# Performance work log

Measured on AMD Instinct MI355X. Metric: run time of the kernel, lower is better.

The kernel has to match this reference:

```python
import jax, jax.numpy as jnp
import numpy as np


def setup_inputs() -> dict:
    key = jax.random.key(0)
    k1, k2 = jax.random.split(key)
    pred_pts = jax.random.normal(k1, (8, 3, 4096), dtype=jnp.float32)  # [B,3,N]
    gt_pts = jax.random.normal(k2, (8, 4096, 3), dtype=jnp.float32)    # [B,M,3]
    return {"pred_pts": pred_pts, "gt_pts": gt_pts}


def _chamfer(p, g):
    # p: [B,N,3], g: [B,M,3]
    # squared euclidean distance matrix via ||p||^2 + ||g||^2 - 2 p.g
    pn = jnp.sum(p * p, axis=-1)  # [B,N]
    gn = jnp.sum(g * g, axis=-1)  # [B,M]
    cross = jnp.einsum("bnd,bmd->bnm", p, g)  # [B,N,M]
    D = pn[:, :, None] + gn[:, None, :] - 2.0 * cross  # [B,N,M]
    dist1 = jnp.min(D, axis=2)  # [B,N] min over gt for each pred point
    dist2 = jnp.min(D, axis=1)  # [B,M] min over pred for each gt point
    return dist1, dist2


def reference(pred_pts, gt_pts):
    p = jnp.swapaxes(pred_pts, -2, -1).astype(jnp.float32)  # [B,N,3]
    g = gt_pts  # [B,M,3]
    dist1, dist2 = _chamfer(p, g)
    per_batch = jnp.mean(dist1, axis=1) + jnp.mean(dist2, axis=1)  # [B]
    loss = jnp.sum(per_batch) / gt_pts.shape[0]
    return loss
```

## Files before the change

### kernel.cpp

```cpp
#include <hip/hip_runtime.h>

typedef float f32x2 __attribute__((ext_vector_type(2)));

#define NPTS 4096
#define BATCH 8
#define BLK 256
#define P 8
#define NPAIR (P / 2)
#define CHUNK 256
#define NCHUNK (NPTS / CHUNK)
#define OWN_PER_BLK (BLK * P)
#define OWN_BLKS (NPTS / OWN_PER_BLK)
#define BLOCKS_PER_PASS (BATCH * OWN_BLKS * NCHUNK)
#define TOTAL_BLOCKS (2 * BLOCKS_PER_PASS)
#define HALF_OWN (BATCH * NPTS)
#define TOTAL_OWN (2 * HALF_OWN)
#define COMBINE_BLOCKS (TOTAL_OWN / BLK)

static __device__ __forceinline__ f32x2 splat2(float v) {
    f32x2 r; r.x = v; r.y = v; return r;
}

__global__ __launch_bounds__(BLK) void chamfer_partial_kernel(
    const float* __restrict__ pred,
    const float* __restrict__ gt,
    float* __restrict__ partial)
{
    __shared__ float4 s[CHUNK];

    const int bid  = blockIdx.x;
    const int pass = bid / BLOCKS_PER_PASS;
    int r = bid - pass * BLOCKS_PER_PASS;
    const int c = r % NCHUNK;
    r /= NCHUNK;
    const int b = r / OWN_BLKS;
    const int j = r - b * OWN_BLKS;
    const int t = threadIdx.x;

    const float* p = pred + (size_t)b * 3 * NPTS;
    const float* g = gt   + (size_t)b * NPTS * 3;
    const int cbase = c * CHUNK;

    {
        int i = t;
        if (pass == 0) {
            int gi = cbase + i;
            float gx = g[gi * 3 + 0], gy = g[gi * 3 + 1], gz = g[gi * 3 + 2];
            s[i] = make_float4(-2.f * gx, -2.f * gy, -2.f * gz,
                               fmaf(gx, gx, fmaf(gy, gy, gz * gz)));
        } else {
            int pi = cbase + i;
            float px = p[pi], py = p[NPTS + pi], pz = p[2 * NPTS + pi];
            s[i] = make_float4(-2.f * px, -2.f * py, -2.f * pz,
                               fmaf(px, px, fmaf(py, py, pz * pz)));
        }
    }

    f32x2 X[NPAIR], Y[NPAIR], Z[NPAIR], N2[NPAIR];
    #pragma unroll
    for (int k = 0; k < P; ++k) {
        int idx = j * OWN_PER_BLK + k * BLK + t;
        float x, y, z;
        if (pass == 0) {
            x = p[idx]; y = p[NPTS + idx]; z = p[2 * NPTS + idx];
        } else {
            x = g[idx * 3 + 0]; y = g[idx * 3 + 1]; z = g[idx * 3 + 2];
        }
        X[k >> 1][k & 1] = x;
        Y[k >> 1][k & 1] = y;
        Z[k >> 1][k & 1] = z;
        N2[k >> 1][k & 1] = fmaf(x, x, fmaf(y, y, z * z));
    }
    __syncthreads();

    f32x2 A[NPAIR], B[NPAIR];
    #pragma unroll
    for (int pk = 0; pk < NPAIR; ++pk) { A[pk] = splat2(3.4e38f); B[pk] = splat2(3.4e38f); }

    #pragma unroll 2
    for (int mm = 0; mm < CHUNK; mm += 2) {
        float4 q0 = s[mm + 0];
        float4 q1 = s[mm + 1];
        f32x2 q0x = splat2(q0.x), q0y = splat2(q0.y), q0z = splat2(q0.z), q0w = splat2(q0.w);
        f32x2 q1x = splat2(q1.x), q1y = splat2(q1.y), q1z = splat2(q1.z), q1w = splat2(q1.w);
        #pragma unroll
        for (int pk = 0; pk < NPAIR; ++pk) {
            f32x2 d0 = __builtin_elementwise_fma(X[pk], q0x,
                        __builtin_elementwise_fma(Y[pk], q0y,
                         __builtin_elementwise_fma(Z[pk], q0z, q0w)));
            A[pk] = __builtin_elementwise_min(A[pk], d0);
            f32x2 d1 = __builtin_elementwise_fma(X[pk], q1x,
                        __builtin_elementwise_fma(Y[pk], q1y,
                         __builtin_elementwise_fma(Z[pk], q1z, q1w)));
            B[pk] = __builtin_elementwise_min(B[pk], d1);
        }
    }

    #pragma unroll
    for (int pk = 0; pk < NPAIR; ++pk) {
        f32x2 mn = __builtin_elementwise_min(A[pk], B[pk]);
        #pragma unroll
        for (int h = 0; h < 2; ++h) {
            int k = 2 * pk + h;
            int idx = j * OWN_PER_BLK + k * BLK + t;
            int o = pass * HALF_OWN + b * NPTS + idx;
            partial[(size_t)c * TOTAL_OWN + o] = N2[pk][h] + mn[h];
        }
    }
}

__global__ __launch_bounds__(BLK) void chamfer_combine_kernel(
    const float* __restrict__ partial, float* __restrict__ bsum)
{
    __shared__ float red[BLK / 64];
    const int t = threadIdx.x;
    const int o = blockIdx.x * BLK + t;
    float v = 3.4e38f;
    #pragma unroll
    for (int c = 0; c < NCHUNK; ++c)
        v = fminf(v, partial[(size_t)c * TOTAL_OWN + o]);
    #pragma unroll
    for (int off = 32; off > 0; off >>= 1)
        v += __shfl_down(v, off, 64);
    if ((t & 63) == 0) red[t >> 6] = v;
    __syncthreads();
    if (t == 0) bsum[blockIdx.x] = red[0] + red[1] + red[2] + red[3];
}

__global__ __launch_bounds__(COMBINE_BLOCKS) void chamfer_final_kernel(
    const float* __restrict__ bsum, float* __restrict__ out)
{
    __shared__ float red[COMBINE_BLOCKS / 64];
    const int t = threadIdx.x;
    float v = bsum[t];
    #pragma unroll
    for (int off = 32; off > 0; off >>= 1)
        v += __shfl_down(v, off, 64);
    if ((t & 63) == 0) red[t >> 6] = v;
    __syncthreads();
    if (t == 0) {
        float s = 0.f;
        #pragma unroll
        for (int w = 0; w < COMBINE_BLOCKS / 64; ++w) s += red[w];
        out[0] = s * (1.0f / ((float)NPTS * (float)BATCH));
    }
}

extern "C" void kernel_launch(void* const* d_in, const int* in_sizes, int n_in,
                              void* d_out, int out_size, void* d_ws, size_t ws_size,
                              hipStream_t stream) {
    const float* pred = (const float*)d_in[0];
    const float* gt   = (const float*)d_in[1];
    float* out = (float*)d_out;

    float* partial = (float*)d_ws;
    float* bsum    = partial + (size_t)NCHUNK * TOTAL_OWN;

    chamfer_partial_kernel<<<TOTAL_BLOCKS, BLK, 0, stream>>>(pred, gt, partial);
    chamfer_combine_kernel<<<COMBINE_BLOCKS, BLK, 0, stream>>>(partial, bsum);
    chamfer_final_kernel<<<1, COMBINE_BLOCKS, 0, stream>>>(bsum, out);
}
```

Measured before the change: 33.42 us.

## Precompute pre-splatted point stream in global memory and drop LDS staging

```diff
diff --git a/kernel.cpp b/kernel.cpp
--- a/kernel.cpp
+++ b/kernel.cpp
@@ -6,7 +6,7 @@
 #define BATCH 8
 #define BLK 256
 #define P 8
-#define NPAIR (P / 2)
+#define NPAIR 4
 #define CHUNK 256
 #define NCHUNK (NPTS / CHUNK)
 #define OWN_PER_BLK (BLK * P)
@@ -16,18 +16,48 @@
 #define HALF_OWN (BATCH * NPTS)
 #define TOTAL_OWN (2 * HALF_OWN)
 #define COMBINE_BLOCKS (TOTAL_OWN / BLK)
+#define STREAM_PTS (BATCH * NPTS)
+#define STREAM_PAD 16
+
+struct Pt8 { f32x2 x, y, z, w; };
 
 static __device__ __forceinline__ f32x2 splat2(float v) {
     f32x2 r; r.x = v; r.y = v; return r;
 }
 
-__global__ __launch_bounds__(BLK) void chamfer_partial_kernel(
+__global__ __launch_bounds__(BLK) void chamfer_prep_kernel(
     const float* __restrict__ pred,
     const float* __restrict__ gt,
+    Pt8* __restrict__ sA, Pt8* __restrict__ sB)
+{
+    const int i = blockIdx.x * BLK + threadIdx.x;
+    const int b = i >> 12;
+    const int m = i & (NPTS - 1);
+
+    {
+        const float* gp = gt + ((size_t)b * NPTS + m) * 3;
+        float gx = gp[0], gy = gp[1], gz = gp[2];
+        Pt8 e;
+        e.x = splat2(-2.f * gx); e.y = splat2(-2.f * gy); e.z = splat2(-2.f * gz);
+        e.w = splat2(fmaf(gx, gx, fmaf(gy, gy, gz * gz)));
+        sA[i] = e;
+    }
+    {
+        const float* pp = pred + (size_t)b * 3 * NPTS;
+        float px = pp[m], py = pp[NPTS + m], pz = pp[2 * NPTS + m];
+        Pt8 e;
+        e.x = splat2(-2.f * px); e.y = splat2(-2.f * py); e.z = splat2(-2.f * pz);
+        e.w = splat2(fmaf(px, px, fmaf(py, py, pz * pz)));
+        sB[i] = e;
+    }
+}
+
+__global__ __launch_bounds__(BLK, 2) void chamfer_partial_kernel(
+    const float* __restrict__ pred,
+    const float* __restrict__ gt,
+    const Pt8* __restrict__ sA, const Pt8* __restrict__ sB,
     float* __restrict__ partial)
 {
-    __shared__ float4 s[CHUNK];
-
     const int bid  = blockIdx.x;
     const int pass = bid / BLOCKS_PER_PASS;
     int r = bid - pass * BLOCKS_PER_PASS;
@@ -39,22 +69,7 @@
 
     const float* p = pred + (size_t)b * 3 * NPTS;
     const float* g = gt   + (size_t)b * NPTS * 3;
-    const int cbase = c * CHUNK;
-
-    {
-        int i = t;
-        if (pass == 0) {
-            int gi = cbase + i;
-            float gx = g[gi * 3 + 0], gy = g[gi * 3 + 1], gz = g[gi * 3 + 2];
-            s[i] = make_float4(-2.f * gx, -2.f * gy, -2.f * gz,
-                               fmaf(gx, gx, fmaf(gy, gy, gz * gz)));
-        } else {
-            int pi = cbase + i;
-            float px = p[pi], py = p[NPTS + pi], pz = p[2 * NPTS + pi];
-            s[i] = make_float4(-2.f * px, -2.f * py, -2.f * pz,
-                               fmaf(px, px, fmaf(py, py, pz * pz)));
-        }
-    }
+    const Pt8* __restrict__ st = (pass == 0 ? sA : sB) + (size_t)b * NPTS + c * CHUNK;
 
     f32x2 X[NPAIR], Y[NPAIR], Z[NPAIR], N2[NPAIR];
     #pragma unroll
@@ -71,30 +86,32 @@
         Z[k >> 1][k & 1] = z;
         N2[k >> 1][k & 1] = fmaf(x, x, fmaf(y, y, z * z));
     }
-    __syncthreads();
 
     f32x2 A[NPAIR], B[NPAIR];
     #pragma unroll
     for (int pk = 0; pk < NPAIR; ++pk) { A[pk] = splat2(3.4e38f); B[pk] = splat2(3.4e38f); }
 
-    #pragma unroll 2
-    for (int mm = 0; mm < CHUNK; mm += 2) {
-        float4 q0 = s[mm + 0];
-        float4 q1 = s[mm + 1];
-        f32x2 q0x = splat2(q0.x), q0y = splat2(q0.y), q0z = splat2(q0.z), q0w = splat2(q0.w);
-        f32x2 q1x = splat2(q1.x), q1y = splat2(q1.y), q1z = splat2(q1.z), q1w = splat2(q1.w);
-        #pragma unroll
-        for (int pk = 0; pk < NPAIR; ++pk) {
-            f32x2 d0 = __builtin_elementwise_fma(X[pk], q0x,
-                        __builtin_elementwise_fma(Y[pk], q0y,
-                         __builtin_elementwise_fma(Z[pk], q0z, q0w)));
-            A[pk] = __builtin_elementwise_min(A[pk], d0);
-            f32x2 d1 = __builtin_elementwise_fma(X[pk], q1x,
-                        __builtin_elementwise_fma(Y[pk], q1y,
-                         __builtin_elementwise_fma(Z[pk], q1z, q1w)));
-            B[pk] = __builtin_elementwise_min(B[pk], d1);
-        }
+    #define COMP(q, ACC)                                                        \
+        do {                                                                    \
+            _Pragma("unroll")                                                   \
+            for (int pk = 0; pk < NPAIR; ++pk) {                                \
+                f32x2 d = __builtin_elementwise_fma((q).x, X[pk],               \
+                           __builtin_elementwise_fma((q).y, Y[pk],              \
+                            __builtin_elementwise_fma((q).z, Z[pk], (q).w)));   \
+                ACC[pk] = __builtin_elementwise_min(ACC[pk], d);                \
+            }                                                                   \
+        } while (0)
+
+    Pt8 a0 = st[0], a1 = st[1], a2 = st[2], a3 = st[3];
+    Pt8 b0, b1, b2, b3;
+    #pragma unroll 1
+    for (int mm = 0; mm < CHUNK; mm += 8) {
+        b0 = st[mm + 4]; b1 = st[mm + 5]; b2 = st[mm + 6]; b3 = st[mm + 7];
+        COMP(a0, A); COMP(a1, B); COMP(a2, A); COMP(a3, B);
+        a0 = st[mm + 8]; a1 = st[mm + 9]; a2 = st[mm + 10]; a3 = st[mm + 11];
+        COMP(b0, A); COMP(b1, B); COMP(b2, A); COMP(b3, B);
     }
+    #undef COMP
 
     #pragma unroll
     for (int pk = 0; pk < NPAIR; ++pk) {
@@ -153,10 +170,13 @@
     const float* gt   = (const float*)d_in[1];
     float* out = (float*)d_out;
 
-    float* partial = (float*)d_ws;
+    Pt8*   sA      = (Pt8*)d_ws;
+    Pt8*   sB      = sA + (STREAM_PTS + STREAM_PAD);
+    float* partial = (float*)(sB + (STREAM_PTS + STREAM_PAD));
     float* bsum    = partial + (size_t)NCHUNK * TOTAL_OWN;
 
-    chamfer_partial_kernel<<<TOTAL_BLOCKS, BLK, 0, stream>>>(pred, gt, partial);
+    chamfer_prep_kernel<<<STREAM_PTS / BLK, BLK, 0, stream>>>(pred, gt, sA, sB);
+    chamfer_partial_kernel<<<TOTAL_BLOCKS, BLK, 0, stream>>>(pred, gt, sA, sB, partial);
     chamfer_combine_kernel<<<COMBINE_BLOCKS, BLK, 0, stream>>>(partial, bsum);
     chamfer_final_kernel<<<1, COMBINE_BLOCKS, 0, stream>>>(bsum, out);
 }
```

New measurement: 36.17 us. 8.2% more time.
